# Kernel tuning notes

Measured on AMD Instinct MI355X. Metric: run time of the kernel, lower is better.

The kernel has to match this reference:

```python
import jax, jax.numpy as jnp
import numpy as np

OUT, IN, R = 8192, 8192, 16
GROUP = 16
SCALING = 16.0 / 16.0  # lora_alpha / r
# nvfp4 (e2m1) code table: 3 low bits magnitude, bit 3 = sign
NVFP4_LUT = jnp.array([0.0, 0.5, 1.0, 1.5, 2.0, 3.0, 4.0, 6.0,
                       -0.0, -0.5, -1.0, -1.5, -2.0, -3.0, -4.0, -6.0],
                      dtype=jnp.float32)


def setup_inputs() -> dict:
    key = jax.random.key(0)
    k1, k2, k3, k4, k5 = jax.random.split(key, 5)
    x = jax.random.normal(k1, (64, IN), dtype=jnp.float32)
    packed_weight = jax.random.randint(k2, (OUT, IN // 2), 0, 256, dtype=jnp.int32).astype(jnp.uint8)
    # effective block scales (global scale already absorbed, as in _load_prequantized_nvfp4)
    weight_block_scales = (jax.random.uniform(k3, (OUT, IN // GROUP), dtype=jnp.float32) + 0.1) * 0.01
    lora_A = jax.random.normal(k4, (R, IN), dtype=jnp.float32) * (1.0 / np.sqrt(IN))
    lora_B = jax.random.normal(k5, (OUT, R), dtype=jnp.float32) * 0.01
    return {"x": x, "packed_weight": packed_weight,
            "weight_block_scales": weight_block_scales,
            "lora_A": lora_A, "lora_B": lora_B}


def _dequant_nvfp4(packed, block_scales):
    # packed: (OUT, IN//2) uint8, two fp4 codes per byte (low nibble = even index)
    low = (packed & 0xF).astype(jnp.int32)
    high = (packed >> 4).astype(jnp.int32)
    codes = jnp.stack([low, high], axis=-1).reshape(packed.shape[0], -1)  # (OUT, IN)
    vals = NVFP4_LUT[codes]
    O, I = vals.shape
    # per-block scale over groups of GROUP along in_features
    W = (vals.reshape(O, I // GROUP, GROUP) * block_scales[:, :, None]).reshape(O, I)
    return W


def reference(x, packed_weight, weight_block_scales, lora_A, lora_B):
    W = _dequant_nvfp4(packed_weight, weight_block_scales)      # (OUT, IN) fp32
    base = x @ W.T                                              # (B, OUT)
    lora = (x @ lora_A.T) @ lora_B.T                            # (B, OUT)
    return base + SCALING * lora
```

## Files before the change

kernel.cpp:

```cpp
#include <hip/hip_runtime.h>
#include <stdint.h>

#define IN_F   8192
#define OUT_F  8192
#define MB     64
#define RANK   16
#define KSPLIT 16
#define KSTEPS 16

typedef _Float16 f16x8 __attribute__((ext_vector_type(8)));
typedef _Float16 f16x2 __attribute__((ext_vector_type(2)));
typedef float    f32x4 __attribute__((ext_vector_type(4)));

__device__ __forceinline__ unsigned pk2h(float a, float b) {
    return __builtin_bit_cast(unsigned, __builtin_amdgcn_cvt_pkrtz(a, b));
}

__device__ __forceinline__ void glds16(const void* gp, void* lp) {
    __builtin_amdgcn_global_load_lds(
        (const __attribute__((address_space(1))) void*)gp,
        (__attribute__((address_space(3))) void*)lp, 16, 0, 0);
}
__device__ __forceinline__ void glds4(const void* gp, void* lp) {
    __builtin_amdgcn_global_load_lds(
        (const __attribute__((address_space(1))) void*)gp,
        (__attribute__((address_space(3))) void*)lp, 4, 0, 0);
}
#define MEMBAR() __asm__ __volatile__("" ::: "memory")

__device__ __forceinline__ f16x8 decode8(unsigned p, unsigned s2) {
    unsigned q  = p >> 4;
    unsigned me = __builtin_amdgcn_perm(0x46444240u, 0x3E3C3800u, p & 0x07070707u);
    unsigned mo = __builtin_amdgcn_perm(0x46444240u, 0x3E3C3800u, q & 0x07070707u);
    unsigned he = ((p & 0x08080808u) << 4) | me;
    unsigned ho = ((q & 0x08080808u) << 4) | mo;
    unsigned bu0 = __builtin_amdgcn_perm(ho, he, 0x040C000Cu);
    unsigned bu1 = __builtin_amdgcn_perm(ho, he, 0x050C010Cu);
    unsigned bu2 = __builtin_amdgcn_perm(ho, he, 0x060C020Cu);
    unsigned bu3 = __builtin_amdgcn_perm(ho, he, 0x070C030Cu);
    f16x2 sv = __builtin_bit_cast(f16x2, s2);
    f16x2 h0 = __builtin_bit_cast(f16x2, bu0) * sv;
    f16x2 h1 = __builtin_bit_cast(f16x2, bu1) * sv;
    f16x2 h2 = __builtin_bit_cast(f16x2, bu2) * sv;
    f16x2 h3 = __builtin_bit_cast(f16x2, bu3) * sv;
    f16x8 b;
    b[0]=h0[0]; b[1]=h0[1]; b[2]=h1[0]; b[3]=h1[1];
    b[4]=h2[0]; b[5]=h2[1]; b[6]=h3[0]; b[7]=h3[1];
    return b;
}

__global__ void detect_kernel(const unsigned* __restrict__ Wp,
                              int* __restrict__ flag, float* __restrict__ t) {
    unsigned v = Wp[threadIdx.x & 63];
    unsigned long long m = __ballot(v > 255u);
    if (threadIdx.x == 0) *flag = (m == 0ull) ? 1 : 0;
    for (int i = threadIdx.x; i < MB * RANK; i += 256) t[i] = 0.f;
}

__global__ __launch_bounds__(256) void prep_kernel(
    const float* __restrict__ x, const float* __restrict__ lora_A,
    uint2* __restrict__ xf2, float* __restrict__ t)
{
    const int m = blockIdx.x, kq = blockIdx.y;
    const int tid = threadIdx.x;
    const int mt = m >> 4, l15 = m & 15;
    float acc[RANK];
#pragma unroll
    for (int r = 0; r < RANK; ++r) acc[r] = 0.f;

    const float4* x4 = (const float4*)(x + (size_t)m * IN_F);
    const float4* A4 = (const float4*)lora_A;
#pragma unroll
    for (int it = 0; it < 2; ++it) {
        int j = kq * 512 + it * 256 + tid;
        float4 xv = x4[j];
        uint2 u;
        u.x = pk2h(xv.x, xv.y);
        u.y = pk2h(xv.z, xv.w);
        int kstep = j >> 3, quad = (j >> 1) & 3, h = j & 1;
        xf2[(size_t)(((kstep * 4 + mt) * 64 + quad * 16 + l15) * 2 + h)] = u;
#pragma unroll
        for (int r = 0; r < RANK; ++r) {
            float4 av = A4[(size_t)r * (IN_F / 4) + j];
            acc[r] += xv.x * av.x + xv.y * av.y + xv.z * av.z + xv.w * av.w;
        }
    }
#pragma unroll
    for (int r = 0; r < RANK; ++r)
#pragma unroll
        for (int off = 32; off > 0; off >>= 1)
            acc[r] += __shfl_down(acc[r], off);

    __shared__ float red[4][RANK];
    int lane = tid & 63, wid = tid >> 6;
    if (lane == 0) {
#pragma unroll
        for (int r = 0; r < RANK; ++r) red[wid][r] = acc[r];
    }
    __syncthreads();
    if (tid < RANK)
        atomicAdd(&t[m * RANK + tid],
                  red[0][tid] + red[1][tid] + red[2][tid] + red[3][tid]);
}

__device__ __forceinline__ float4 lora4(const float* __restrict__ t, int m,
                                        const float* __restrict__ lora_B, int n4) {
    const float4* t4 = (const float4*)(t + m * RANK);
    float4 ta = t4[0], tb = t4[1], tc = t4[2], td = t4[3];
    float4 o;
    float* op = (float*)&o;
#pragma unroll
    for (int j = 0; j < 4; ++j) {
        const float4* B4 = (const float4*)(lora_B + (size_t)(n4 + j) * RANK);
        float4 b0 = B4[0], b1 = B4[1], b2 = B4[2], b3 = B4[3];
        op[j] = ta.x * b0.x + ta.y * b0.y + ta.z * b0.z + ta.w * b0.w
              + tb.x * b1.x + tb.y * b1.y + tb.z * b1.z + tb.w * b1.w
              + tc.x * b2.x + tc.y * b2.y + tc.z * b2.z + tc.w * b2.w
              + td.x * b3.x + td.y * b3.y + td.z * b3.z + td.w * b3.w;
    }
    return o;
}

__global__ __launch_bounds__(256) void lora_kernel(
    const float* __restrict__ t, const float* __restrict__ lora_B,
    float* __restrict__ out)
{
    const int gid = blockIdx.x * 256 + threadIdx.x;
    ((float4*)out)[gid] = lora4(t, gid >> 11, lora_B, (gid & 2047) * 4);
}

__global__ __launch_bounds__(256) void finish_kernel(
    const float* __restrict__ partial, const float* __restrict__ t,
    const float* __restrict__ lora_B, float* __restrict__ out)
{
    const int gid = blockIdx.x * 256 + threadIdx.x;
    float4 p = {0.f, 0.f, 0.f, 0.f};
#pragma unroll
    for (int ksp = 0; ksp < KSPLIT; ++ksp) {
        float4 v = ((const float4*)partial)[(size_t)ksp * (MB * OUT_F / 4) + gid];
        p.x += v.x; p.y += v.y; p.z += v.z; p.w += v.w;
    }
    float4 l = lora4(t, gid >> 11, lora_B, (gid & 2047) * 4);
    p.x += l.x; p.y += l.y; p.z += l.z; p.w += l.w;
    ((float4*)out)[gid] = p;
}

template<int FMT, int ATOMIC>
__global__ __launch_bounds__(512, 4) void main_kernel(
    const void*  __restrict__ Wpv,
    const float* __restrict__ scales,
    const uint4* __restrict__ xf4,
    const int*   __restrict__ flag,
    float*       __restrict__ dst)
{
    if (*flag != FMT) return;

    __shared__ __align__(16) char xs[65536];
    __shared__ __align__(16) char wl[65536];

    const int tid = threadIdx.x;
    const int lane = tid & 63, w = tid >> 6;
    const int l15 = lane & 15, quad = lane >> 4, qh = quad >> 1;
    const int ks = blockIdx.x;
    const int n0 = blockIdx.y * 256 + w * 32;
    const int row = n0 + l15;

    unsigned sreg[2][KSTEPS];
    {
        const float4* sp0 = (const float4*)(scales + (size_t)row * (IN_F / 16) + ks * 32);
        const float4* sp1 = (const float4*)(scales + (size_t)(row + 16) * (IN_F / 16) + ks * 32);
#pragma unroll
        for (int nt = 0; nt < 2; ++nt) {
            const float4* sp = nt ? sp1 : sp0;
#pragma unroll
            for (int i = 0; i < 8; ++i) {
                float4 v = sp[i];
                float a = qh ? v.y : v.x, b = qh ? v.w : v.z;
                sreg[nt][2 * i]     = pk2h(a, a);
                sreg[nt][2 * i + 1] = pk2h(b, b);
            }
        }
    }

    {
        const uint4* gsrc = xf4 + (size_t)ks * (KSTEPS * 4 * 64);
#pragma unroll
        for (int i = 0; i < 8; ++i) {
            int idx = i * 512 + tid;
            uint4 v = gsrc[idx];
            *(uint4*)&xs[(size_t)idx * 16] = v;
        }
    }
    __syncthreads();

    f32x4 acc[4][2];
#pragma unroll
    for (int mt = 0; mt < 4; ++mt)
#pragma unroll
        for (int nt = 0; nt < 2; ++nt)
            acc[mt][nt] = (f32x4){0.f, 0.f, 0.f, 0.f};

    char* wlw = &wl[(size_t)w * 8192];

#define ISSUE(c, buf)                                                        \
    do {                                                                     \
        _Pragma("unroll") for (int j = 0; j < 2; ++j)                        \
        _Pragma("unroll") for (int nt = 0; nt < 2; ++nt) {                   \
            size_t e = (size_t)(row + nt * 16) * 1024                        \
                       + (ks * 64 + ((c) * 2 + j) * 4 + quad);               \
            char* ldst = &wlw[(size_t)((buf) * 4 + j * 2 + nt) * 1024];      \
            if (FMT == 1) glds16((const char*)Wpv + e * 16, ldst);           \
            else          glds4 ((const char*)Wpv + e * 4,  ldst);           \
        }                                                                    \
    } while (0)

    ISSUE(0, 0);
    ISSUE(1, 1);

#pragma unroll
    for (int c = 0; c < 8; ++c) {
        const int buf = c & 1;
        MEMBAR();
        if (c < 7) __builtin_amdgcn_s_waitcnt(0x0F74);
        else       __builtin_amdgcn_s_waitcnt(0x0F70);
        MEMBAR();
#pragma unroll
        for (int j = 0; j < 2; ++j) {
            const int s = c * 2 + j;
            f16x8 afr[4];
#pragma unroll
            for (int mt = 0; mt < 4; ++mt)
                afr[mt] = *(const f16x8*)&xs[(size_t)((s * 4 + mt) * 64 + lane) * 16];
#pragma unroll
            for (int nt = 0; nt < 2; ++nt) {
                const char* slot = &wlw[(size_t)(buf * 4 + j * 2 + nt) * 1024];
                unsigned p;
                if (FMT == 1) {
                    uint4 u = *(const uint4*)(slot + (size_t)lane * 16);
                    p = u.x | (u.y << 8) | (u.z << 16) | (u.w << 24);
                } else {
                    p = *(const unsigned*)(slot + (size_t)lane * 4);
                }
                f16x8 b = decode8(p, sreg[nt][s]);
#pragma unroll
                for (int mt = 0; mt < 4; ++mt)
                    acc[mt][nt] = __builtin_amdgcn_mfma_f32_16x16x32_f16(
                        afr[mt], b, acc[mt][nt], 0, 0, 0);
            }
        }
        if (c < 6) { MEMBAR(); ISSUE(c + 2, buf); }
    }
#undef ISSUE

    if (ATOMIC == 0) {
        float* pb = dst + (size_t)ks * (MB * OUT_F);
#pragma unroll
        for (int mt = 0; mt < 4; ++mt)
#pragma unroll
            for (int nt = 0; nt < 2; ++nt)
#pragma unroll
                for (int r = 0; r < 4; ++r)
                    pb[(size_t)(mt * 16 + quad * 4 + r) * OUT_F + n0 + nt * 16 + l15]
                        = acc[mt][nt][r];
    } else {
#pragma unroll
        for (int mt = 0; mt < 4; ++mt)
#pragma unroll
            for (int nt = 0; nt < 2; ++nt)
#pragma unroll
                for (int r = 0; r < 4; ++r)
                    atomicAdd(&dst[(size_t)(mt * 16 + quad * 4 + r) * OUT_F
                                   + n0 + nt * 16 + l15], acc[mt][nt][r]);
    }
}

extern "C" void kernel_launch(void* const* d_in, const int* in_sizes, int n_in,
                              void* d_out, int out_size, void* d_ws, size_t ws_size,
                              hipStream_t stream)
{
    (void)in_sizes; (void)n_in; (void)out_size;
    const float* x      = (const float*)d_in[0];
    const void*  Wp     = (const void*)d_in[1];
    const float* scales = (const float*)d_in[2];
    const float* lora_A = (const float*)d_in[3];
    const float* lora_B = (const float*)d_in[4];
    float* out = (float*)d_out;

    char* ws = (char*)d_ws;
    int*   flag    = (int*)ws;
    float* t       = (float*)(ws + 4096);
    uint2* xf      = (uint2*)(ws + 65536);
    float* partial = (float*)(ws + (2u << 20));

    const bool big_ws = ws_size >= ((size_t)34 << 20);

    detect_kernel<<<1, 256, 0, stream>>>((const unsigned*)Wp, flag, t);
    prep_kernel<<<dim3(64, 4), 256, 0, stream>>>(x, lora_A, xf, t);

    if (big_ws) {
        main_kernel<1, 0><<<dim3(KSPLIT, 32), 512, 0, stream>>>(
            Wp, scales, (const uint4*)xf, flag, partial);
        main_kernel<0, 0><<<dim3(KSPLIT, 32), 512, 0, stream>>>(
            Wp, scales, (const uint4*)xf, flag, partial);
        finish_kernel<<<(MB * OUT_F / 4) / 256, 256, 0, stream>>>(
            partial, t, lora_B, out);
    } else {
        lora_kernel<<<(MB * OUT_F / 4) / 256, 256, 0, stream>>>(t, lora_B, out);
        main_kernel<1, 1><<<dim3(KSPLIT, 32), 512, 0, stream>>>(
            Wp, scales, (const uint4*)xf, flag, out);
        main_kernel<0, 1><<<dim3(KSPLIT, 32), 512, 0, stream>>>(
            Wp, scales, (const uint4*)xf, flag, out);
    }
}
```

Measured before the change: 240.9 us.

## Repack weights into fragment-ordered layout and drop LDS staging in main kernel

Adds a repack kernel that reads the packed weights (either uint8 stored as uint32 or raw bytes) and writes them into a workspace buffer already in MFMA fragment order, with two rows per uint2. The main kernel then reads weights and activations straight from global memory with coalesced loads instead of staging through LDS with async loads, and uses smaller 256-thread blocks over twice as many row tiles. This removes the duplicate format-specific launches and the LDS pipeline, but adds a full extra read and write of the weight matrix every call, which is a large new memory cost for a bandwidth-bound GEMV-like op.

```diff
diff --git a/kernel.cpp b/kernel.cpp
--- a/kernel.cpp
+++ b/kernel.cpp
@@ -6,7 +6,6 @@
 #define MB     64
 #define RANK   16
 #define KSPLIT 16
-#define KSTEPS 16
 
 typedef _Float16 f16x8 __attribute__((ext_vector_type(8)));
 typedef _Float16 f16x2 __attribute__((ext_vector_type(2)));
@@ -15,18 +14,6 @@
 __device__ __forceinline__ unsigned pk2h(float a, float b) {
     return __builtin_bit_cast(unsigned, __builtin_amdgcn_cvt_pkrtz(a, b));
 }
-
-__device__ __forceinline__ void glds16(const void* gp, void* lp) {
-    __builtin_amdgcn_global_load_lds(
-        (const __attribute__((address_space(1))) void*)gp,
-        (__attribute__((address_space(3))) void*)lp, 16, 0, 0);
-}
-__device__ __forceinline__ void glds4(const void* gp, void* lp) {
-    __builtin_amdgcn_global_load_lds(
-        (const __attribute__((address_space(1))) void*)gp,
-        (__attribute__((address_space(3))) void*)lp, 4, 0, 0);
-}
-#define MEMBAR() __asm__ __volatile__("" ::: "memory")
 
 __device__ __forceinline__ f16x8 decode8(unsigned p, unsigned s2) {
     unsigned q  = p >> 4;
@@ -49,12 +36,43 @@
     return b;
 }
 
-__global__ void detect_kernel(const unsigned* __restrict__ Wp,
-                              int* __restrict__ flag, float* __restrict__ t) {
-    unsigned v = Wp[threadIdx.x & 63];
-    unsigned long long m = __ballot(v > 255u);
-    if (threadIdx.x == 0) *flag = (m == 0ull) ? 1 : 0;
-    for (int i = threadIdx.x; i < MB * RANK; i += 256) t[i] = 0.f;
+__global__ __launch_bounds__(256) void repack_kernel(
+    const void* __restrict__ Wpv, unsigned* __restrict__ W2,
+    float* __restrict__ t)
+{
+    const int tid = threadIdx.x;
+    const unsigned U = blockIdx.x * 256 + tid;
+
+    unsigned v = ((const unsigned*)Wpv)[tid & 63];
+    const bool fmt1 = (__ballot(v > 255u) == 0ull);
+
+    if (blockIdx.x == 0) {
+        for (int i = tid; i < MB * RANK; i += 256) t[i] = 0.f;
+    }
+
+    const int lane = U & 63;
+    const int s    = (U >> 6) & 15;
+    const int w    = (U >> 10) & 3;
+    const int by   = (U >> 12) & 63;
+    const int ks   = (U >> 18) & 15;
+    const int l15  = lane & 15, quad = lane >> 4;
+    const int row0 = by * 128 + w * 32 + l15;
+    const int e    = ks * 64 + s * 4 + quad;
+
+    unsigned d0, d1;
+    if (fmt1) {
+        const uint4* in4 = (const uint4*)Wpv;
+        uint4 a = in4[(size_t)row0 * 1024 + e];
+        uint4 b = in4[(size_t)(row0 + 16) * 1024 + e];
+        d0 = (a.x & 0xFFu) | ((a.y & 0xFFu) << 8) | ((a.z & 0xFFu) << 16) | (a.w << 24);
+        d1 = (b.x & 0xFFu) | ((b.y & 0xFFu) << 8) | ((b.z & 0xFFu) << 16) | (b.w << 24);
+    } else {
+        const unsigned* in1 = (const unsigned*)Wpv;
+        d0 = in1[(size_t)row0 * 1024 + e];
+        d1 = in1[(size_t)(row0 + 16) * 1024 + e];
+    }
+    uint2 o; o.x = d0; o.y = d1;
+    ((uint2*)W2)[U] = o;
 }
 
 __global__ __launch_bounds__(256) void prep_kernel(
@@ -145,53 +163,33 @@
     ((float4*)out)[gid] = p;
 }
 
-template<int FMT, int ATOMIC>
-__global__ __launch_bounds__(512, 4) void main_kernel(
-    const void*  __restrict__ Wpv,
-    const float* __restrict__ scales,
-    const uint4* __restrict__ xf4,
-    const int*   __restrict__ flag,
-    float*       __restrict__ dst)
-{
-    if (*flag != FMT) return;
-
-    __shared__ __align__(16) char xs[65536];
-    __shared__ __align__(16) char wl[65536];
-
+template<int ATOMIC>
+__global__ __launch_bounds__(256, 4) void main3_kernel(
+    const unsigned* __restrict__ W2,
+    const float*    __restrict__ scales,
+    const uint4*    __restrict__ xf4,
+    float*          __restrict__ dst)
+{
     const int tid = threadIdx.x;
     const int lane = tid & 63, w = tid >> 6;
     const int l15 = lane & 15, quad = lane >> 4, qh = quad >> 1;
-    const int ks = blockIdx.x;
-    const int n0 = blockIdx.y * 256 + w * 32;
+    const int ks = blockIdx.x, by = blockIdx.y;
+    const int n0 = by * 128 + w * 32;
     const int row = n0 + l15;
 
-    unsigned sreg[2][KSTEPS];
-    {
-        const float4* sp0 = (const float4*)(scales + (size_t)row * (IN_F / 16) + ks * 32);
-        const float4* sp1 = (const float4*)(scales + (size_t)(row + 16) * (IN_F / 16) + ks * 32);
-#pragma unroll
-        for (int nt = 0; nt < 2; ++nt) {
-            const float4* sp = nt ? sp1 : sp0;
-#pragma unroll
-            for (int i = 0; i < 8; ++i) {
-                float4 v = sp[i];
-                float a = qh ? v.y : v.x, b = qh ? v.w : v.z;
-                sreg[nt][2 * i]     = pk2h(a, a);
-                sreg[nt][2 * i + 1] = pk2h(b, b);
-            }
+    unsigned sreg[2][16];
+#pragma unroll
+    for (int nt = 0; nt < 2; ++nt) {
+        const float4* sp = (const float4*)(scales + (size_t)(row + nt * 16) * (IN_F / 16)
+                                           + ks * 32);
+#pragma unroll
+        for (int i = 0; i < 8; ++i) {
+            float4 v = sp[i];
+            float a = qh ? v.y : v.x, b = qh ? v.w : v.z;
+            sreg[nt][2 * i]     = pk2h(a, a);
+            sreg[nt][2 * i + 1] = pk2h(b, b);
         }
     }
-
-    {
-        const uint4* gsrc = xf4 + (size_t)ks * (KSTEPS * 4 * 64);
-#pragma unroll
-        for (int i = 0; i < 8; ++i) {
-            int idx = i * 512 + tid;
-            uint4 v = gsrc[idx];
-            *(uint4*)&xs[(size_t)idx * 16] = v;
-        }
-    }
-    __syncthreads();
 
     f32x4 acc[4][2];
 #pragma unroll
@@ -200,57 +198,27 @@
         for (int nt = 0; nt < 2; ++nt)
             acc[mt][nt] = (f32x4){0.f, 0.f, 0.f, 0.f};
 
-    char* wlw = &wl[(size_t)w * 8192];
-
-#define ISSUE(c, buf)                                                        \
-    do {                                                                     \
-        _Pragma("unroll") for (int j = 0; j < 2; ++j)                        \
-        _Pragma("unroll") for (int nt = 0; nt < 2; ++nt) {                   \
-            size_t e = (size_t)(row + nt * 16) * 1024                        \
-                       + (ks * 64 + ((c) * 2 + j) * 4 + quad);               \
-            char* ldst = &wlw[(size_t)((buf) * 4 + j * 2 + nt) * 1024];      \
-            if (FMT == 1) glds16((const char*)Wpv + e * 16, ldst);           \
-            else          glds4 ((const char*)Wpv + e * 4,  ldst);           \
-        }                                                                    \
-    } while (0)
-
-    ISSUE(0, 0);
-    ISSUE(1, 1);
-
-#pragma unroll
-    for (int c = 0; c < 8; ++c) {
-        const int buf = c & 1;
-        MEMBAR();
-        if (c < 7) __builtin_amdgcn_s_waitcnt(0x0F74);
-        else       __builtin_amdgcn_s_waitcnt(0x0F70);
-        MEMBAR();
-#pragma unroll
-        for (int j = 0; j < 2; ++j) {
-            const int s = c * 2 + j;
-            f16x8 afr[4];
+    const uint2* wp = (const uint2*)W2
+                    + (((size_t)(ks * 64 + by) * 4 + w) * 16) * 64 + lane;
+    const uint4* xp = xf4 + (size_t)ks * 4096 + lane;
+
+#pragma unroll
+    for (int s = 0; s < 16; ++s) {
+        uint2 u = wp[s * 64];
+        f16x8 afr[4];
+#pragma unroll
+        for (int mt = 0; mt < 4; ++mt)
+            afr[mt] = __builtin_bit_cast(f16x8, xp[(s * 4 + mt) * 64]);
+#pragma unroll
+        for (int nt = 0; nt < 2; ++nt) {
+            unsigned p = nt ? u.y : u.x;
+            f16x8 b = decode8(p, sreg[nt][s]);
 #pragma unroll
             for (int mt = 0; mt < 4; ++mt)
-                afr[mt] = *(const f16x8*)&xs[(size_t)((s * 4 + mt) * 64 + lane) * 16];
-#pragma unroll
-            for (int nt = 0; nt < 2; ++nt) {
-                const char* slot = &wlw[(size_t)(buf * 4 + j * 2 + nt) * 1024];
-                unsigned p;
-                if (FMT == 1) {
-                    uint4 u = *(const uint4*)(slot + (size_t)lane * 16);
-                    p = u.x | (u.y << 8) | (u.z << 16) | (u.w << 24);
-                } else {
-                    p = *(const unsigned*)(slot + (size_t)lane * 4);
-                }
-                f16x8 b = decode8(p, sreg[nt][s]);
-#pragma unroll
-                for (int mt = 0; mt < 4; ++mt)
-                    acc[mt][nt] = __builtin_amdgcn_mfma_f32_16x16x32_f16(
-                        afr[mt], b, acc[mt][nt], 0, 0, 0);
-            }
+                acc[mt][nt] = __builtin_amdgcn_mfma_f32_16x16x32_f16(
+                    afr[mt], b, acc[mt][nt], 0, 0, 0);
         }
-        if (c < 6) { MEMBAR(); ISSUE(c + 2, buf); }
-    }
-#undef ISSUE
+    }
 
     if (ATOMIC == 0) {
         float* pb = dst + (size_t)ks * (MB * OUT_F);
@@ -287,28 +255,24 @@
     float* out = (float*)d_out;
 
     char* ws = (char*)d_ws;
-    int*   flag    = (int*)ws;
     float* t       = (float*)(ws + 4096);
     uint2* xf      = (uint2*)(ws + 65536);
     float* partial = (float*)(ws + (2u << 20));
-
-    const bool big_ws = ws_size >= ((size_t)34 << 20);
-
-    detect_kernel<<<1, 256, 0, stream>>>((const unsigned*)Wp, flag, t);
+    const bool full = ws_size >= ((size_t)67 << 20);
+    unsigned* W2 = full ? (unsigned*)(ws + (34u << 20))
+                        : (unsigned*)(ws + (2u << 20));
+
+    repack_kernel<<<(OUT_F * (IN_F / 8) / 2) / 256, 256, 0, stream>>>(Wp, W2, t);
     prep_kernel<<<dim3(64, 4), 256, 0, stream>>>(x, lora_A, xf, t);
 
-    if (big_ws) {
-        main_kernel<1, 0><<<dim3(KSPLIT, 32), 512, 0, stream>>>(
-            Wp, scales, (const uint4*)xf, flag, partial);
-        main_kernel<0, 0><<<dim3(KSPLIT, 32), 512, 0, stream>>>(
-            Wp, scales, (const uint4*)xf, flag, partial);
+    if (full) {
+        main3_kernel<0><<<dim3(KSPLIT, 64), 256, 0, stream>>>(
+            W2, scales, (const uint4*)xf, partial);
         finish_kernel<<<(MB * OUT_F / 4) / 256, 256, 0, stream>>>(
             partial, t, lora_B, out);
     } else {
         lora_kernel<<<(MB * OUT_F / 4) / 256, 256, 0, stream>>>(t, lora_B, out);
-        main_kernel<1, 1><<<dim3(KSPLIT, 32), 512, 0, stream>>>(
-            Wp, scales, (const uint4*)xf, flag, out);
-        main_kernel<0, 1><<<dim3(KSPLIT, 32), 512, 0, stream>>>(
-            Wp, scales, (const uint4*)xf, flag, out);
-    }
-}
+        main3_kernel<1><<<dim3(KSPLIT, 64), 256, 0, stream>>>(
+            W2, scales, (const uint4*)xf, out);
+    }
+}
```

Result: slower. 260.0 us (+8.0%).
